# Performance work log

Hardware: AMD Instinct MI355X
Metric: run time of the kernel (lower is better)

## Reference

```python
import jax, jax.numpy as jnp
import numpy as np
import itertools

NUM_HEADS = 8
KEY_DIM = 32
ATTN_D = 128  # attn_ratio * key_dim
BN_EPS = 1e-5


def _build_idxs(rx=16, rz=8, tn=1):
    points = list(itertools.product(range(rx), range(rx)))
    for i in range(tn):
        points += list(itertools.product(range(rx + rz * i, rx + rz * (i + 1)),
                                         range(rx + rz * i, rx + rz * (i + 1))))
    offsets = {}
    idxs = []
    for p1 in points:
        for p2 in points:
            off = (abs(p1[0] - p2[0]), abs(p1[1] - p2[1]))
            if off not in offsets:
                offsets[off] = len(offsets)
            idxs.append(offsets[off])
    N = len(points)
    return np.asarray(idxs, dtype=np.int64).reshape(N, N), len(offsets)


def _bn_train(x2d, gamma, beta):
    # BatchNorm1d in training mode: batch mean / biased variance over dim 0
    m = jnp.mean(x2d, axis=0)
    v = jnp.var(x2d, axis=0)
    return (x2d - m) * jax.lax.rsqrt(v + BN_EPS) * gamma + beta


def setup_inputs() -> dict:
    key = jax.random.key(0)
    ks = jax.random.split(key, 4)
    idxs_np, n_off = _build_idxs()  # (320,320), 560
    B, N, C = 128, idxs_np.shape[0], 256
    h = NUM_HEADS * (2 * KEY_DIM + ATTN_D)  # 1536
    dh = NUM_HEADS * ATTN_D  # 1024
    return {
        "x": jax.random.normal(ks[0], (B, N, C), dtype=jnp.float32),
        "Wqkv": jax.random.normal(ks[1], (h, C), dtype=jnp.float32) * 0.02,
        "g1": jnp.ones((h,), jnp.float32),
        "b1": jnp.zeros((h,), jnp.float32),
        "ab": jax.random.normal(ks[2], (NUM_HEADS, n_off), dtype=jnp.float32) * 0.02,
        "Wproj": jax.random.normal(ks[3], (C, dh), dtype=jnp.float32) * 0.02,
        "g2": jnp.ones((C,), jnp.float32),
        "b2": jnp.zeros((C,), jnp.float32),
        "idxs": jnp.asarray(idxs_np),
    }


def reference(x, Wqkv, g1, b1, ab, Wproj, g2, b2, idxs):
    B, N, C = x.shape
    scale = KEY_DIM ** -0.5
    # qkv projection (Linear no-bias) + BatchNorm1d over flattened (B*N, h)
    qkv = jnp.einsum('bnc,hc->bnh', x, Wqkv)
    qkv = _bn_train(qkv.reshape(B * N, -1), g1, b1).reshape(B, N, NUM_HEADS, 2 * KEY_DIM + ATTN_D)
    q = qkv[..., :KEY_DIM]
    k = qkv[..., KEY_DIM:2 * KEY_DIM]
    v = qkv[..., 2 * KEY_DIM:]
    bias = ab[:, idxs]  # gather -> (H, N, N)
    attn = jnp.einsum('bnhd,bmhd->bhnm', q, k) * scale + bias[None]
    attn = jax.nn.softmax(attn, axis=-1)
    out = jnp.einsum('bhnm,bmhd->bnhd', attn, v).reshape(B, N, NUM_HEADS * ATTN_D)
    out = jax.nn.gelu(out, approximate=False)  # activation() before proj
    out = jnp.einsum('bnd,cd->bnc', out, Wproj)
    out = _bn_train(out.reshape(B * N, -1), g2, b2).reshape(B, N, C)
    return out
```

## Files before the change

kernel.cpp:

```cpp
#include <hip/hip_runtime.h>
#include <hip/hip_bf16.h>

#define B_ 128
#define N_ 320
#define C_ 256
#define H_ 8
#define HQKV 1536
#define DH 1024
#define MROWS 40960
#define EPS 1e-5f
#define SCALE 0.17677669529663687f
#define LOG2E 1.4426950408889634f

typedef __attribute__((ext_vector_type(4))) float f32x4;
typedef __attribute__((ext_vector_type(8))) short short8_t;
typedef __attribute__((ext_vector_type(4))) short short4_t;

__device__ inline float bf2f(unsigned short u) { return __uint_as_float(((unsigned)u) << 16); }
__device__ inline unsigned short f2bf(float f) {
    unsigned u = __float_as_uint(f);
    u += 0x7FFF + ((u >> 16) & 1);
    return (unsigned short)(u >> 16);
}
__device__ inline unsigned int f2bf2(float a, float b) {
    __hip_bfloat162 h2 = __float22bfloat162_rn(make_float2(a, b));
    return *(unsigned int*)&h2;
}

__device__ inline float gelu_f(float v) {
    float v2 = v * v;
    float w = fmaf(v2, 0.044715f, 1.0f);
    float z = v * w * (-2.3022098f);
    float e = __builtin_amdgcn_exp2f(z);
    return v * __builtin_amdgcn_rcpf(1.0f + e);
}

#define GLD16(gp, lp)                                                                  \
    __builtin_amdgcn_global_load_lds((const __attribute__((address_space(1))) void*)(gp), \
                                     (__attribute__((address_space(3))) void*)(lp), 16, 0, 0)

__global__ void conv_all(const float* __restrict__ x, const float* __restrict__ wqkv,
                         const float* __restrict__ wproj, unsigned short* __restrict__ xb,
                         unsigned short* __restrict__ wqb, unsigned short* __restrict__ wpb) {
    int i = blockIdx.x * 256 + threadIdx.x;
    const float* src;
    unsigned short* dst;
    int off;
    if (i < 2621440) { src = x; dst = xb; off = i; }
    else if (i < 2719744) { src = wqkv; dst = wqb; off = i - 2621440; }
    else if (i < 2785280) { src = wproj; dst = wpb; off = i - 2719744; }
    else return;
    f32x4 v = ((const f32x4*)src)[off];
    short4_t o;
#pragma unroll
    for (int j = 0; j < 4; ++j) o[j] = (short)f2bf(v[j]);
    ((short4_t*)dst)[off] = o;
}

__global__ __launch_bounds__(256) void gemm_qkv(const unsigned short* __restrict__ A,
                                                const unsigned short* __restrict__ Bm,
                                                unsigned short* __restrict__ qkB,
                                                unsigned short* __restrict__ vT,
                                                float* __restrict__ sum1, float* __restrict__ sumsq1) {
    __shared__ unsigned short lA[128 * 32];
    __shared__ unsigned short lB[128 * 32];
    const int tid = threadIdx.x;
    const int lane = tid & 63, wid = tid >> 6;
    const int wm = wid >> 1, wn = wid & 1;
    const int lr = lane & 15, g = lane >> 4, lk = g * 8;
    const int orig = blockIdx.y * 12 + blockIdx.x;
    const int id2 = (orig & 7) * 480 + (orig >> 3);
    const int m0 = (id2 / 12) * 128, n0 = (id2 % 12) * 128;
    const int wb0 = tid & 192;
    f32x4 acc[4][4] = {};
    for (int k0 = 0; k0 < 256; k0 += 32) {
        __syncthreads();
#pragma unroll
        for (int j = 0; j < 2; ++j) {
            int idx = j * 256 + tid;
            int wb = j * 256 + wb0;
            GLD16(&A[(size_t)(m0 + (idx >> 2)) * 256 + k0 + (idx & 3) * 8], &lA[(size_t)wb * 8]);
            GLD16(&Bm[(size_t)(n0 + (idx >> 2)) * 256 + k0 + (idx & 3) * 8], &lB[(size_t)wb * 8]);
        }
        __syncthreads();
        short8_t af[4], bfr[4];
#pragma unroll
        for (int i = 0; i < 4; ++i) af[i] = *(short8_t*)&lA[(wm * 64 + i * 16 + lr) * 32 + lk];
#pragma unroll
        for (int j = 0; j < 4; ++j) bfr[j] = *(short8_t*)&lB[(wn * 64 + j * 16 + lr) * 32 + lk];
#pragma unroll
        for (int i = 0; i < 4; ++i)
#pragma unroll
            for (int j = 0; j < 4; ++j)
                acc[i][j] = __builtin_amdgcn_mfma_f32_16x16x32_bf16(af[i], bfr[j], acc[i][j], 0, 0, 0);
    }
    int hhj[4], cmj[4];
#pragma unroll
    for (int j = 0; j < 4; ++j) {
        int col = n0 + wn * 64 + j * 16 + lr;
        hhj[j] = col / 192;
        cmj[j] = col - hhj[j] * 192;
    }
    float cs[4] = {0.f, 0.f, 0.f, 0.f}, css[4] = {0.f, 0.f, 0.f, 0.f};
#pragma unroll
    for (int i = 0; i < 4; ++i) {
        int rowbase = m0 + wm * 64 + i * 16 + g * 4;
        int bq = rowbase / 320;
        int n = rowbase - bq * 320;
#pragma unroll
        for (int j = 0; j < 4; ++j) {
            float v0 = acc[i][j][0], v1 = acc[i][j][1], v2 = acc[i][j][2], v3 = acc[i][j][3];
            cs[j] += (v0 + v1) + (v2 + v3);
            css[j] += (v0 * v0 + v1 * v1) + (v2 * v2 + v3 * v3);
            if (cmj[j] < 64) {
                unsigned short* qp = &qkB[((size_t)(bq * 8 + hhj[j]) * 320 + n) * 64 + cmj[j]];
                qp[0] = f2bf(v0); qp[64] = f2bf(v1); qp[128] = f2bf(v2); qp[192] = f2bf(v3);
            } else {
                short4_t o;
                o[0] = (short)f2bf(v0); o[1] = (short)f2bf(v1);
                o[2] = (short)f2bf(v2); o[3] = (short)f2bf(v3);
                *(short4_t*)&vT[((size_t)(bq * 8 + hhj[j]) * 128 + (cmj[j] - 64)) * 320 + n] = o;
            }
        }
    }
    __syncthreads();
    float* red_s = (float*)lA;
    float* red_ss = (float*)lB;
#pragma unroll
    for (int j = 0; j < 4; ++j) {
        int c = wn * 64 + j * 16 + lr;
        red_s[(wm * 4 + g) * 128 + c] = cs[j];
        red_ss[(wm * 4 + g) * 128 + c] = css[j];
    }
    __syncthreads();
    if (tid < 128) {
        float s = 0.f;
#pragma unroll
        for (int u = 0; u < 8; ++u) s += red_s[u * 128 + tid];
        atomicAdd(&sum1[n0 + tid], s);
    } else {
        int c = tid - 128;
        float s = 0.f;
#pragma unroll
        for (int u = 0; u < 8; ++u) s += red_ss[u * 128 + c];
        atomicAdd(&sumsq1[n0 + c], s);
    }
}

__global__ __launch_bounds__(256) void gemm_proj(const unsigned short* __restrict__ A,
                                                 const unsigned short* __restrict__ Bm,
                                                 float* __restrict__ Cout,
                                                 float* __restrict__ sum2, float* __restrict__ sumsq2) {
    __shared__ unsigned short lA[64 * 32];
    __shared__ unsigned short lB[128 * 32];
    const int tid = threadIdx.x;
    const int lane = tid & 63, wid = tid >> 6;
    const int wm = wid >> 1, wn = wid & 1;
    const int lr = lane & 15, g = lane >> 4, lk = g * 8;
    const int m0 = blockIdx.y * 64, n0 = blockIdx.x * 128;
    const int wb0 = tid & 192;
    f32x4 acc[2][4] = {};
    for (int k0 = 0; k0 < 1024; k0 += 32) {
        __syncthreads();
        GLD16(&A[(size_t)(m0 + (tid >> 2)) * 1024 + k0 + (tid & 3) * 8], &lA[(size_t)wb0 * 8]);
        GLD16(&Bm[(size_t)(n0 + (tid >> 2)) * 1024 + k0 + (tid & 3) * 8], &lB[(size_t)wb0 * 8]);
        GLD16(&Bm[(size_t)(n0 + 64 + (tid >> 2)) * 1024 + k0 + (tid & 3) * 8], &lB[2048 + (size_t)wb0 * 8]);
        __syncthreads();
        short8_t af[2], bfr[4];
#pragma unroll
        for (int i = 0; i < 2; ++i) af[i] = *(short8_t*)&lA[(wm * 32 + i * 16 + lr) * 32 + lk];
#pragma unroll
        for (int j = 0; j < 4; ++j) bfr[j] = *(short8_t*)&lB[(wn * 64 + j * 16 + lr) * 32 + lk];
#pragma unroll
        for (int i = 0; i < 2; ++i)
#pragma unroll
            for (int j = 0; j < 4; ++j)
                acc[i][j] = __builtin_amdgcn_mfma_f32_16x16x32_bf16(af[i], bfr[j], acc[i][j], 0, 0, 0);
    }
    float cs[4] = {0.f, 0.f, 0.f, 0.f}, css[4] = {0.f, 0.f, 0.f, 0.f};
#pragma unroll
    for (int i = 0; i < 2; ++i) {
#pragma unroll
        for (int r = 0; r < 4; ++r) {
            int row = m0 + wm * 32 + i * 16 + g * 4 + r;
#pragma unroll
            for (int j = 0; j < 4; ++j) {
                float val = acc[i][j][r];
                cs[j] += val;
                css[j] += val * val;
                Cout[(size_t)row * 256 + n0 + wn * 64 + j * 16 + lr] = val;
            }
        }
    }
    __syncthreads();
    float* red_s = (float*)lB;
    float* red_ss = (float*)lB + 1024;
#pragma unroll
    for (int j = 0; j < 4; ++j) {
        int c = wn * 64 + j * 16 + lr;
        red_s[(wm * 4 + g) * 128 + c] = cs[j];
        red_ss[(wm * 4 + g) * 128 + c] = css[j];
    }
    __syncthreads();
    if (tid < 128) {
        float s = 0.f;
#pragma unroll
        for (int u = 0; u < 8; ++u) s += red_s[u * 128 + tid];
        atomicAdd(&sum2[n0 + tid], s);
    } else {
        int c = tid - 128;
        float s = 0.f;
#pragma unroll
        for (int u = 0; u < 8; ++u) s += red_ss[u * 128 + c];
        atomicAdd(&sumsq2[n0 + c], s);
    }
}

__global__ void bn_finalize(const float* __restrict__ sum, const float* __restrict__ sumsq,
                            const float* __restrict__ g, const float* __restrict__ b,
                            float* __restrict__ scale, float* __restrict__ shift, int C, float invM) {
    int c = blockIdx.x * 256 + threadIdx.x;
    if (c < C) {
        float mean = sum[c] * invM;
        float var = sumsq[c] * invM - mean * mean;
        float sc = g[c] * rsqrtf(var + EPS);
        scale[c] = sc;
        shift[c] = b[c] - mean * sc;
    }
}

__global__ void prep_w(const float* __restrict__ scale1, const float* __restrict__ shift1,
                       float* __restrict__ wq, float* __restrict__ w2) {
    int c = threadIdx.x;
    if (c < 256) {
        int h = c >> 5, cc = c & 31;
        int qch = h * 192 + cc, kch = qch + 32;
        wq[c] = scale1[qch] * scale1[kch] * (SCALE * LOG2E);
        w2[c] = shift1[qch] * scale1[kch] * (SCALE * LOG2E);
    }
}

__global__ void uk_kernel(const unsigned short* __restrict__ qkB, const float* __restrict__ w2,
                          float* __restrict__ uk) {
    int idx = blockIdx.x * 256 + threadIdx.x;
    if (idx < 128 * 8 * 320) {
        int bh = idx / 320;
        int h = bh & 7;
        const unsigned short* kp = &qkB[(size_t)idx * 64 + 32];
        float s = 0.f;
#pragma unroll
        for (int c4 = 0; c4 < 4; ++c4) {
            short8_t kk = *(const short8_t*)&kp[c4 * 8];
#pragma unroll
            for (int j = 0; j < 8; ++j) s += bf2f((unsigned short)kk[j]) * w2[(h << 5) + c4 * 8 + j];
        }
        uk[idx] = s;
    }
}

__global__ void bias_build(const float* __restrict__ ab, const int* __restrict__ idxs,
                           float* __restrict__ biasf, int n_off) {
    int i = blockIdx.x * 256 + threadIdx.x;
    if (i < H_ * N_ * N_) {
        int h = i / (N_ * N_);
        int r = i % (N_ * N_);
        biasf[i] = ab[h * n_off + idxs[r]] * LOG2E;
    }
}

__global__ __launch_bounds__(256) void attn_kernel(const unsigned short* __restrict__ qkB,
                                                   const unsigned short* __restrict__ vT,
                                                   const float* __restrict__ wq,
                                                   const float* __restrict__ uk,
                                                   const float* __restrict__ biasf,
                                                   const float* __restrict__ scale1,
                                                   const float* __restrict__ shift1,
                                                   unsigned short* __restrict__ attnout) {
    __shared__ unsigned short Plds[4][10][16][40];
    __shared__ float sums[64];
    const int tid = threadIdx.x;
    const int lane = tid & 63, wid = tid >> 6;
    const int lr = lane & 15, g = lane >> 4;
    const int h = blockIdx.x;
    const int b = blockIdx.y / 5, qt = blockIdx.y % 5;
    const int bh = b * 8 + h;

    const int qrow = qt * 64 + wid * 16 + lr;
    short8_t qraw = *(const short8_t*)&qkB[((size_t)bh * 320 + qrow) * 64 + g * 8];
    short8_t aq;
#pragma unroll
    for (int j = 0; j < 8; ++j)
        aq[j] = (short)f2bf(bf2f((unsigned short)qraw[j]) * wq[(h << 5) + g * 8 + j]);

    const unsigned short* Kbase = &qkB[(size_t)bh * 320 * 64 + 32 + g * 8];
    f32x4 sacc[20];
#pragma unroll
    for (int t = 0; t < 20; ++t) {
        short8_t bk = *(const short8_t*)&Kbase[(size_t)(t * 16 + lr) * 64];
        f32x4 z = {};
        sacc[t] = __builtin_amdgcn_mfma_f32_16x16x32_bf16(bk, aq, z, 0, 0, 0);
    }

    const float* brow = &biasf[(size_t)h * 102400 + (size_t)qrow * 320];
    const float* ukrow = &uk[(size_t)bh * 320];
    float sumr = 0.f;
#pragma unroll
    for (int t = 0; t < 20; ++t) {
        int mb = t * 16 + g * 4;
        f32x4 b4 = *(const f32x4*)&brow[mb];
        f32x4 uk4 = *(const f32x4*)&ukrow[mb];
        float p0 = __builtin_amdgcn_exp2f(sacc[t][0] + uk4[0] + b4[0]);
        float p1 = __builtin_amdgcn_exp2f(sacc[t][1] + uk4[1] + b4[1]);
        float p2 = __builtin_amdgcn_exp2f(sacc[t][2] + uk4[2] + b4[2]);
        float p3 = __builtin_amdgcn_exp2f(sacc[t][3] + uk4[3] + b4[3]);
        sumr += (p0 + p1) + (p2 + p3);
        *(uint2*)&Plds[wid][t >> 1][lr][((t & 1) << 4) + (g << 2)] =
            make_uint2(f2bf2(p0, p1), f2bf2(p2, p3));
    }
    sumr += __shfl_xor(sumr, 16);
    sumr += __shfl_xor(sumr, 32);
    if (lane < 16) sums[wid * 16 + lr] = sumr;
    __syncthreads();

    const unsigned short* Vb = &vT[(size_t)bh * 128 * 320 + g * 8];
    f32x4 oacc[4][2] = {};
#pragma unroll
    for (int t = 0; t < 10; ++t) {
        short8_t bv0 = *(const short8_t*)&Vb[(size_t)(wid * 32 + lr) * 320 + t * 32];
        short8_t bv1 = *(const short8_t*)&Vb[(size_t)(wid * 32 + 16 + lr) * 320 + t * 32];
#pragma unroll
        for (int qw = 0; qw < 4; ++qw) {
            short8_t ap = *(short8_t*)&Plds[qw][t][lr][g * 8];
            oacc[qw][0] = __builtin_amdgcn_mfma_f32_16x16x32_bf16(ap, bv0, oacc[qw][0], 0, 0, 0);
            oacc[qw][1] = __builtin_amdgcn_mfma_f32_16x16x32_bf16(ap, bv1, oacc[qw][1], 0, 0, 0);
        }
    }

    float svv[2], tvv[2];
#pragma unroll
    for (int dtl = 0; dtl < 2; ++dtl) {
        int ch = h * 192 + 64 + wid * 32 + dtl * 16 + lr;
        svv[dtl] = scale1[ch];
        tvv[dtl] = shift1[ch];
    }
#pragma unroll
    for (int qw = 0; qw < 4; ++qw) {
#pragma unroll
        for (int r = 0; r < 4; ++r) {
            float inv = __builtin_amdgcn_rcpf(sums[qw * 16 + g * 4 + r]);
            size_t nrow = (size_t)b * 320 + qt * 64 + qw * 16 + g * 4 + r;
#pragma unroll
            for (int dtl = 0; dtl < 2; ++dtl) {
                float v = oacc[qw][dtl][r] * inv * svv[dtl] + tvv[dtl];
                attnout[nrow * 1024 + h * 128 + wid * 32 + dtl * 16 + lr] = f2bf(gelu_f(v));
            }
        }
    }
}

__global__ void bn_apply(float* __restrict__ out, const float* __restrict__ scale,
                         const float* __restrict__ shift) {
    int i = blockIdx.x * 256 + threadIdx.x;
    const int total = MROWS * C_ / 4;
    for (; i < total; i += gridDim.x * 256) {
        f32x4 v = *(const f32x4*)&out[(size_t)i * 4];
        int c = (i * 4) & 255;
        f32x4 o;
#pragma unroll
        for (int j = 0; j < 4; ++j) o[j] = v[j] * scale[c + j] + shift[c + j];
        *(f32x4*)&out[(size_t)i * 4] = o;
    }
}

extern "C" void kernel_launch(void* const* d_in, const int* in_sizes, int n_in,
                              void* d_out, int out_size, void* d_ws, size_t ws_size,
                              hipStream_t stream) {
    const float* x = (const float*)d_in[0];
    const float* Wqkv = (const float*)d_in[1];
    const float* g1 = (const float*)d_in[2];
    const float* b1 = (const float*)d_in[3];
    const float* ab = (const float*)d_in[4];
    const float* Wproj = (const float*)d_in[5];
    const float* g2 = (const float*)d_in[6];
    const float* b2 = (const float*)d_in[7];
    const int* idxs = (const int*)d_in[8];
    const int n_off = in_sizes[4] / H_;

    char* ws = (char*)d_ws;
    unsigned short* qkB = (unsigned short*)ws;
    unsigned short* vT = (unsigned short*)(ws + 41943040);
    unsigned short* attnout = (unsigned short*)(ws + 125829120);
    unsigned short* xb = attnout;
    float* biasf = (float*)(ws + 209715200);
    float* uk = (float*)(ws + 212992000);
    unsigned short* wqb = (unsigned short*)(ws + 214302720);
    unsigned short* wpb = (unsigned short*)(ws + 215089152);
    float* stats = (float*)(ws + 215613440);
    float* sum1 = stats;
    float* sumsq1 = stats + 1536;
    float* sum2 = stats + 3072;
    float* sumsq2 = sum2 + 256;
    float* scale1 = sumsq2 + 256;
    float* shift1 = scale1 + 1536;
    float* scale2 = shift1 + 1536;
    float* shift2 = scale2 + 256;
    float* wq = shift2 + 256;
    float* w2 = wq + 256;

    hipMemsetAsync(stats, 0, 3584 * 4, stream);
    conv_all<<<dim3(10880), 256, 0, stream>>>(x, Wqkv, Wproj, xb, wqb, wpb);
    bias_build<<<dim3(3200), 256, 0, stream>>>(ab, idxs, biasf, n_off);
    gemm_qkv<<<dim3(12, 320), 256, 0, stream>>>(xb, wqb, qkB, vT, sum1, sumsq1);
    bn_finalize<<<dim3(6), 256, 0, stream>>>(sum1, sumsq1, g1, b1, scale1, shift1, 1536, 1.0f / MROWS);
    prep_w<<<dim3(1), 256, 0, stream>>>(scale1, shift1, wq, w2);
    uk_kernel<<<dim3(1280), 256, 0, stream>>>(qkB, w2, uk);
    attn_kernel<<<dim3(8, 640), 256, 0, stream>>>(qkB, vT, wq, uk, biasf, scale1, shift1, attnout);
    gemm_proj<<<dim3(2, 640), 256, 0, stream>>>(attnout, wpb, (float*)d_out, sum2, sumsq2);
    bn_finalize<<<dim3(1), 256, 0, stream>>>(sum2, sumsq2, g2, b2, scale2, shift2, 256, 1.0f / MROWS);
    bn_apply<<<dim3(2048), 256, 0, stream>>>((float*)d_out, scale2, shift2);
}
```

Measured before the change: 329.0 us.

## Keep softmax probabilities in registers and fuse PV MFMA per key chunk

Rewrites the attention kernel so each wave computes S^T tiles with permuted key rows. The exponentiated probabilities then land directly in the MFMA operand layout for the P·V product, which removes the LDS staging buffer, the per-row sums array and the block barrier. The PV product is interleaved chunk by chunk with the QK product, and each wave now owns all 128 output dims for its 16 query rows, so the epilogue writes packed 4-element stores. It also adds a min-blocks hint to launch_bounds. The trade-off is that each wave loads all of V itself, with no cross-wave sharing, and register pressure rises under the occupancy hint.

```diff
diff --git a/kernel.cpp b/kernel.cpp
--- a/kernel.cpp
+++ b/kernel.cpp
@@ -268,16 +268,14 @@
     }
 }
 
-__global__ __launch_bounds__(256) void attn_kernel(const unsigned short* __restrict__ qkB,
-                                                   const unsigned short* __restrict__ vT,
-                                                   const float* __restrict__ wq,
-                                                   const float* __restrict__ uk,
-                                                   const float* __restrict__ biasf,
-                                                   const float* __restrict__ scale1,
-                                                   const float* __restrict__ shift1,
-                                                   unsigned short* __restrict__ attnout) {
-    __shared__ unsigned short Plds[4][10][16][40];
-    __shared__ float sums[64];
+__global__ __launch_bounds__(256, 4) void attn_kernel(const unsigned short* __restrict__ qkB,
+                                                      const unsigned short* __restrict__ vT,
+                                                      const float* __restrict__ wq,
+                                                      const float* __restrict__ uk,
+                                                      const float* __restrict__ biasf,
+                                                      const float* __restrict__ scale1,
+                                                      const float* __restrict__ shift1,
+                                                      unsigned short* __restrict__ attnout) {
     const int tid = threadIdx.x;
     const int lane = tid & 63, wid = tid >> 6;
     const int lr = lane & 15, g = lane >> 4;
@@ -292,69 +290,57 @@
     for (int j = 0; j < 8; ++j)
         aq[j] = (short)f2bf(bf2f((unsigned short)qraw[j]) * wq[(h << 5) + g * 8 + j]);
 
-    const unsigned short* Kbase = &qkB[(size_t)bh * 320 * 64 + 32 + g * 8];
-    f32x4 sacc[20];
-#pragma unroll
-    for (int t = 0; t < 20; ++t) {
-        short8_t bk = *(const short8_t*)&Kbase[(size_t)(t * 16 + lr) * 64];
-        f32x4 z = {};
-        sacc[t] = __builtin_amdgcn_mfma_f32_16x16x32_bf16(bk, aq, z, 0, 0, 0);
-    }
-
+    const int krow_loc = ((lr >> 2) << 3) + (lr & 3);
+    const unsigned short* Kbase = &qkB[((size_t)bh * 320 + krow_loc) * 64 + 32 + g * 8];
     const float* brow = &biasf[(size_t)h * 102400 + (size_t)qrow * 320];
     const float* ukrow = &uk[(size_t)bh * 320];
+    const unsigned short* Vb = &vT[((size_t)bh * 128 + lr) * 320 + g * 8];
+
+    f32x4 oacc[8] = {};
     float sumr = 0.f;
 #pragma unroll
-    for (int t = 0; t < 20; ++t) {
-        int mb = t * 16 + g * 4;
-        f32x4 b4 = *(const f32x4*)&brow[mb];
-        f32x4 uk4 = *(const f32x4*)&ukrow[mb];
-        float p0 = __builtin_amdgcn_exp2f(sacc[t][0] + uk4[0] + b4[0]);
-        float p1 = __builtin_amdgcn_exp2f(sacc[t][1] + uk4[1] + b4[1]);
-        float p2 = __builtin_amdgcn_exp2f(sacc[t][2] + uk4[2] + b4[2]);
-        float p3 = __builtin_amdgcn_exp2f(sacc[t][3] + uk4[3] + b4[3]);
-        sumr += (p0 + p1) + (p2 + p3);
-        *(uint2*)&Plds[wid][t >> 1][lr][((t & 1) << 4) + (g << 2)] =
-            make_uint2(f2bf2(p0, p1), f2bf2(p2, p3));
-    }
+    for (int ch = 0; ch < 10; ++ch) {
+        uint2 packs[2];
+#pragma unroll
+        for (int hf = 0; hf < 2; ++hf) {
+            short8_t bk = *(const short8_t*)&Kbase[(size_t)(ch * 32 + hf * 4) * 64];
+            f32x4 z = {};
+            f32x4 s4 = __builtin_amdgcn_mfma_f32_16x16x32_bf16(bk, aq, z, 0, 0, 0);
+            int mb = ch * 32 + g * 8 + hf * 4;
+            f32x4 b4 = *(const f32x4*)&brow[mb];
+            f32x4 uk4 = *(const f32x4*)&ukrow[mb];
+            float p0 = __builtin_amdgcn_exp2f(s4[0] + uk4[0] + b4[0]);
+            float p1 = __builtin_amdgcn_exp2f(s4[1] + uk4[1] + b4[1]);
+            float p2 = __builtin_amdgcn_exp2f(s4[2] + uk4[2] + b4[2]);
+            float p3 = __builtin_amdgcn_exp2f(s4[3] + uk4[3] + b4[3]);
+            sumr += (p0 + p1) + (p2 + p3);
+            packs[hf] = make_uint2(f2bf2(p0, p1), f2bf2(p2, p3));
+        }
+        uint4 bf4 = make_uint4(packs[0].x, packs[0].y, packs[1].x, packs[1].y);
+        short8_t pfrag = *(short8_t*)&bf4;
+#pragma unroll
+        for (int dt = 0; dt < 8; ++dt) {
+            short8_t av = *(const short8_t*)&Vb[(size_t)(dt * 16) * 320 + ch * 32];
+            oacc[dt] = __builtin_amdgcn_mfma_f32_16x16x32_bf16(av, pfrag, oacc[dt], 0, 0, 0);
+        }
+    }
+
     sumr += __shfl_xor(sumr, 16);
     sumr += __shfl_xor(sumr, 32);
-    if (lane < 16) sums[wid * 16 + lr] = sumr;
-    __syncthreads();
-
-    const unsigned short* Vb = &vT[(size_t)bh * 128 * 320 + g * 8];
-    f32x4 oacc[4][2] = {};
-#pragma unroll
-    for (int t = 0; t < 10; ++t) {
-        short8_t bv0 = *(const short8_t*)&Vb[(size_t)(wid * 32 + lr) * 320 + t * 32];
-        short8_t bv1 = *(const short8_t*)&Vb[(size_t)(wid * 32 + 16 + lr) * 320 + t * 32];
-#pragma unroll
-        for (int qw = 0; qw < 4; ++qw) {
-            short8_t ap = *(short8_t*)&Plds[qw][t][lr][g * 8];
-            oacc[qw][0] = __builtin_amdgcn_mfma_f32_16x16x32_bf16(ap, bv0, oacc[qw][0], 0, 0, 0);
-            oacc[qw][1] = __builtin_amdgcn_mfma_f32_16x16x32_bf16(ap, bv1, oacc[qw][1], 0, 0, 0);
-        }
-    }
-
-    float svv[2], tvv[2];
-#pragma unroll
-    for (int dtl = 0; dtl < 2; ++dtl) {
-        int ch = h * 192 + 64 + wid * 32 + dtl * 16 + lr;
-        svv[dtl] = scale1[ch];
-        tvv[dtl] = shift1[ch];
-    }
-#pragma unroll
-    for (int qw = 0; qw < 4; ++qw) {
-#pragma unroll
-        for (int r = 0; r < 4; ++r) {
-            float inv = __builtin_amdgcn_rcpf(sums[qw * 16 + g * 4 + r]);
-            size_t nrow = (size_t)b * 320 + qt * 64 + qw * 16 + g * 4 + r;
-#pragma unroll
-            for (int dtl = 0; dtl < 2; ++dtl) {
-                float v = oacc[qw][dtl][r] * inv * svv[dtl] + tvv[dtl];
-                attnout[nrow * 1024 + h * 128 + wid * 32 + dtl * 16 + lr] = f2bf(gelu_f(v));
-            }
-        }
+    float inv = __builtin_amdgcn_rcpf(sumr);
+
+    size_t nrow = (size_t)b * 320 + qrow;
+    unsigned short* obase = &attnout[nrow * 1024 + h * 128 + g * 4];
+#pragma unroll
+    for (int dt = 0; dt < 8; ++dt) {
+        int chnl = h * 192 + 64 + dt * 16 + g * 4;
+        f32x4 sv4 = *(const f32x4*)&scale1[chnl];
+        f32x4 tv4 = *(const f32x4*)&shift1[chnl];
+        float o0 = gelu_f(oacc[dt][0] * inv * sv4[0] + tv4[0]);
+        float o1 = gelu_f(oacc[dt][1] * inv * sv4[1] + tv4[1]);
+        float o2 = gelu_f(oacc[dt][2] * inv * sv4[2] + tv4[2]);
+        float o3 = gelu_f(oacc[dt][3] * inv * sv4[3] + tv4[3]);
+        *(uint2*)&obase[dt * 16] = make_uint2(f2bf2(o0, o1), f2bf2(o2, o3));
     }
 }
 
```

Measured after the change: 472.1 us. +43.5%, slower.
